# Kernel optimization log

Measured on AMD Instinct MI355X. Metric: run time of the kernel, lower is better.

The kernel has to match this reference:

```python
import jax, jax.numpy as jnp
import numpy as np
import math

# Model dims (from init_kwargs + mamba_ssm Mamba2 defaults)
D_MODEL = 1024
EXPAND = 2
HEADDIM = 64
D_STATE = 64
D_CONV = 4
NGROUPS = 1
D_INNER = EXPAND * D_MODEL            # 2048
NHEADS = D_INNER // HEADDIM           # 32
CONV_DIM = D_INNER + 2 * NGROUPS * D_STATE   # 2176
D_IN_PROJ = 2 * D_INNER + 2 * NGROUPS * D_STATE + NHEADS  # 4256
BATCH, SEQLEN = 4, 2048
RMS_EPS = 1.1920929e-07   # torch.finfo(float32).eps (nn.RMSNorm eps=None)
GNORM_EPS = 1e-5          # mamba_ssm RMSNormGated eps


def _rmsnorm(x, w, eps):
    return x * jax.lax.rsqrt(jnp.mean(x * x, axis=-1, keepdims=True) + eps) * w


def setup_inputs() -> dict:
    key = jax.random.key(0)
    ks = jax.random.split(key, 8)
    x = jax.random.normal(ks[0], (BATCH, SEQLEN, D_MODEL), jnp.float32)
    # router MLP (Linear(d_model,32) -> SiLU -> Linear(32,3))
    r_w1 = jax.random.normal(ks[1], (32, D_MODEL), jnp.float32) / math.sqrt(D_MODEL)
    r_b1 = jnp.zeros((32,), jnp.float32)
    r_w2 = jax.random.normal(ks[2], (3, 32), jnp.float32) / math.sqrt(32)
    r_b2 = jnp.zeros((3,), jnp.float32)
    # Mamba2 params
    in_proj_w = jax.random.normal(ks[3], (D_IN_PROJ, D_MODEL), jnp.float32) / math.sqrt(D_MODEL)
    conv_w = jax.random.normal(ks[4], (CONV_DIM, D_CONV), jnp.float32) * 0.2
    conv_b = jnp.zeros((CONV_DIM,), jnp.float32)
    dt_bias = jax.random.normal(ks[5], (NHEADS,), jnp.float32) * 0.1
    # OrthoSSM multi-scale override: A_log[i] = log(0.001 * 2**i)
    A_log = jnp.log(0.001 * (2.0 ** jnp.arange(NHEADS, dtype=jnp.float32)))
    D_param = jnp.ones((NHEADS,), jnp.float32)
    gnorm_w = jnp.ones((D_INNER,), jnp.float32)
    out_proj_w = jax.random.normal(ks[6], (D_MODEL, D_INNER), jnp.float32) / math.sqrt(D_INNER)
    norm_w = jnp.ones((D_MODEL,), jnp.float32)
    return {"x": x, "norm_w": norm_w, "r_w1": r_w1, "r_b1": r_b1, "r_w2": r_w2,
            "r_b2": r_b2, "in_proj_w": in_proj_w, "conv_w": conv_w, "conv_b": conv_b,
            "dt_bias": dt_bias, "A_log": A_log, "D_param": D_param,
            "gnorm_w": gnorm_w, "out_proj_w": out_proj_w}


def _forward(x, norm_w, r_w1, r_b1, r_w2, r_b2, in_proj_w, conv_w, conv_b,
             dt_bias, A_log, D_param, gnorm_w, out_proj_w):
    B, S, Dm = x.shape
    x_norm = _rmsnorm(x, norm_w, RMS_EPS)
    # --- router: mean-pool -> tiny MLP -> softmax over 3 tiers ---
    h = jax.nn.silu(x_norm.mean(axis=1) @ r_w1.T + r_b1)
    probs = jax.nn.softmax(h @ r_w2.T + r_b2, axis=-1)   # [B,3]
    p_fast = probs[:, 0][:, None, None]
    p_mamba = (probs[:, 1] + probs[:, 2])[:, None, None]
    # --- Mamba2(x_norm) ---
    zxbcdt = x_norm @ in_proj_w.T                         # [B,S,4256]
    z, xBC, dt = jnp.split(zxbcdt, [D_INNER, D_INNER + CONV_DIM], axis=-1)
    # causal depthwise conv1d (kernel 4) + SiLU
    conv = jax.lax.conv_general_dilated(
        xBC.transpose(0, 2, 1), conv_w[:, None, :], (1,), [(D_CONV - 1, 0)],
        feature_group_count=CONV_DIM)                      # [B,CONV_DIM,S]
    xBC = jax.nn.silu(conv.transpose(0, 2, 1) + conv_b)    # [B,S,CONV_DIM]
    xh, Bmat, Cmat = jnp.split(xBC, [D_INNER, D_INNER + NGROUPS * D_STATE], axis=-1)
    xh = xh.reshape(B, S, NHEADS, HEADDIM)                 # [B,S,H,P]
    dt = jax.nn.softplus(dt + dt_bias)                     # [B,S,H]
    A = -jnp.exp(A_log)                                    # [H]
    dA = jnp.exp(dt * A)                                   # [B,S,H]

    def step(hstate, inp):
        dA_t, dt_t, x_t, B_t, C_t = inp
        # hstate: [B,H,P,N]
        hstate = hstate * dA_t[..., None, None] \
                 + (dt_t[..., None] * x_t)[..., None] * B_t[:, None, None, :]
        y_t = jnp.einsum('bhpn,bn->bhp', hstate, C_t)
        return hstate, y_t

    h0 = jnp.zeros((B, NHEADS, HEADDIM, D_STATE), x.dtype)
    xs = (dA.transpose(1, 0, 2), dt.transpose(1, 0, 2), xh.transpose(1, 0, 2, 3),
          Bmat.transpose(1, 0, 2), Cmat.transpose(1, 0, 2))
    _, ys = jax.lax.scan(step, h0, xs)                     # [S,B,H,P]
    y = ys.transpose(1, 0, 2, 3) + D_param[:, None] * xh   # D skip connection
    y = y.reshape(B, S, D_INNER)
    # gated RMSNorm: norm(y * silu(z)) * weight
    yg = y * jax.nn.silu(z)
    yg = _rmsnorm(yg, gnorm_w, GNORM_EPS)
    mamba_out = yg @ out_proj_w.T                          # [B,S,D]
    out = p_fast * x_norm + p_mamba * mamba_out
    return x + out


def reference(x, norm_w, r_w1, r_b1, r_w2, r_b2, in_proj_w, conv_w, conv_b,
              dt_bias, A_log, D_param, gnorm_w, out_proj_w):
    return _forward(x, norm_w, r_w1, r_b1, r_w2, r_b2, in_proj_w, conv_w, conv_b,
                    dt_bias, A_log, D_param, gnorm_w, out_proj_w)
```

## Files before the change

### kernel.cpp

```cpp
#include <hip/hip_runtime.h>
#include <math.h>

typedef __bf16 bf16;
typedef __bf16 bf16x8 __attribute__((ext_vector_type(8)));
typedef __bf16 bf16x4 __attribute__((ext_vector_type(4)));
typedef float f32x4 __attribute__((ext_vector_type(4)));

#define DEV static __device__ __forceinline__
#define AS1 __attribute__((address_space(1)))
#define AS3 __attribute__((address_space(3)))

constexpr int kBatch = 4, kSeq = 2048, kDModel = 1024;
constexpr int kDInner = 2048, kHeads = 32;
constexpr int kConvDim = 2176, kDInProj = 4256, kNPad1 = 4352;
constexpr int kRows = kBatch * kSeq;
constexpr int kChunk = 64, kNChunk = kSeq / kChunk;
constexpr float kRmsEps = 1.1920929e-07f;
constexpr float kGnEps = 1e-5f;

DEV float siluf(float x) { return x / (1.f + expf(-x)); }

DEV float block_reduce_sum(float v, float* red, int tid) {
#pragma unroll
  for (int m = 1; m < 64; m <<= 1) v += __shfl_xor(v, m);
  if ((tid & 63) == 0) red[tid >> 6] = v;
  __syncthreads();
  return red[0] + red[1] + red[2] + red[3];
}

__global__ __launch_bounds__(256) void k_rmsnorm(const float* __restrict__ x,
                                                 const float* __restrict__ nw,
                                                 bf16* __restrict__ xnb,
                                                 float* __restrict__ rs) {
  const int row = blockIdx.x;
  const int tid = threadIdx.x;
  float4 v = ((const float4*)(x + (size_t)row * kDModel))[tid];
  __shared__ float red[4];
  float ss = block_reduce_sum(v.x * v.x + v.y * v.y + v.z * v.z + v.w * v.w, red, tid);
  float scale = rsqrtf(ss * (1.f / kDModel) + kRmsEps);
  if (tid == 0) rs[row] = scale;
  float4 wv = ((const float4*)nw)[tid];
  bf16x4 ov;
  ov[0] = (bf16)(v.x * scale * wv.x);
  ov[1] = (bf16)(v.y * scale * wv.y);
  ov[2] = (bf16)(v.z * scale * wv.z);
  ov[3] = (bf16)(v.w * scale * wv.w);
  *(bf16x4*)(xnb + (size_t)row * kDModel + tid * 4) = ov;
}

__global__ __launch_bounds__(128) void k_pool1(const bf16* __restrict__ xnb,
                                               float* __restrict__ part) {
  const int g = blockIdx.x, b = blockIdx.y;
  const int tid = threadIdx.x;
  const bf16* base = xnb + ((size_t)b * kSeq + (size_t)g * 32) * kDModel + tid * 8;
  float acc[8] = {0, 0, 0, 0, 0, 0, 0, 0};
  for (int r = 0; r < 32; ++r) {
    bf16x8 v = *(const bf16x8*)(base + (size_t)r * kDModel);
#pragma unroll
    for (int j = 0; j < 8; ++j) acc[j] += (float)v[j];
  }
  float* o = part + ((size_t)b * 64 + g) * kDModel + tid * 8;
#pragma unroll
  for (int j = 0; j < 8; ++j) o[j] = acc[j];
}

__global__ __launch_bounds__(256) void k_pool2(const float* __restrict__ part,
                                               float* __restrict__ mean) {
  const int idx = blockIdx.x * 256 + threadIdx.x;
  const int b = idx >> 10, d = idx & 1023;
  float s = 0.f;
  for (int g = 0; g < 64; ++g) s += part[((size_t)b * 64 + g) * kDModel + d];
  mean[idx] = s * (1.f / kSeq);
}

__global__ __launch_bounds__(128) void k_router(const float* __restrict__ mean,
                                                const float* __restrict__ w1,
                                                const float* __restrict__ b1,
                                                const float* __restrict__ w2,
                                                const float* __restrict__ b2,
                                                float* __restrict__ pfm) {
  __shared__ float hbuf[4][32];
  __shared__ float logit[4][3];
  const int t = threadIdx.x;
  {
    int b = t >> 5, j = t & 31;
    float s = b1[j];
    for (int d = 0; d < kDModel; ++d) s += mean[b * kDModel + d] * w1[j * kDModel + d];
    hbuf[b][j] = siluf(s);
  }
  __syncthreads();
  if (t < 12) {
    int b = t / 3, k = t % 3;
    float s = b2[k];
    for (int j = 0; j < 32; ++j) s += hbuf[b][j] * w2[k * 32 + j];
    logit[b][k] = s;
  }
  __syncthreads();
  if (t < 4) {
    float m = fmaxf(logit[t][0], fmaxf(logit[t][1], logit[t][2]));
    float e0 = expf(logit[t][0] - m), e1 = expf(logit[t][1] - m), e2 = expf(logit[t][2] - m);
    float inv = 1.f / (e0 + e1 + e2);
    pfm[t] = e0 * inv;
    pfm[4 + t] = (e1 + e2) * inv;
  }
}

__global__ __launch_bounds__(256) void k_castpad_w1(const float* __restrict__ w,
                                                    bf16* __restrict__ wb) {
  const size_t idx = (size_t)blockIdx.x * 256 + threadIdx.x;
  const int row = (int)(idx >> 10);
  wb[idx] = (bf16)(row < kDInProj ? w[idx] : 0.f);
}

__global__ __launch_bounds__(256) void k_cast_w2(const float* __restrict__ w,
                                                 const float* __restrict__ gw,
                                                 bf16* __restrict__ wb) {
  const size_t i4 = (size_t)blockIdx.x * 256 + threadIdx.x;
  const int k4 = (int)((i4 * 4) & (kDInner - 1));
  float4 v = ((const float4*)w)[i4];
  float4 g = *(const float4*)(gw + k4);
  bf16x4 o;
  o[0] = (bf16)(v.x * g.x); o[1] = (bf16)(v.y * g.y);
  o[2] = (bf16)(v.z * g.z); o[3] = (bf16)(v.w * g.w);
  ((bf16x4*)wb)[i4] = o;
}

template <int WM, int WN, int NF, bool FUSE>
__global__ __launch_bounds__(WM * WN * 64, 4) void k_gemm(
    const bf16* __restrict__ A, const bf16* __restrict__ B,
    bf16* __restrict__ Cb, const float* __restrict__ xres,
    const float* __restrict__ rs, const float* __restrict__ nw,
    const float* __restrict__ pfm, const float* __restrict__ rs2,
    float* __restrict__ outf, int K, int Nreal, int ldc, int ntn) {
  constexpr int THREADS = WM * WN * 64;
  constexpr int BM = WM * 64;
  constexpr int BN = WN * NF * 16;
  constexpr int NA = (BM * 4) / THREADS;
  constexpr int NB = (BN * 4) / THREADS;
  constexpr int ASZ = (BM / 2) * 64;
  constexpr int BSZ = (BN / 2) * 64;
  __shared__ __align__(16) bf16 lds[2 * ASZ + 2 * BSZ];
  const int tid = threadIdx.x;
  const int lane = tid & 63, wid = tid >> 6;
  const int wr = wid / WN, wc = wid % WN;
  const int lr = lane & 15, kb = lane >> 4;
  const int cpx = (int)gridDim.x >> 3;
  const int bid = ((int)blockIdx.x & 7) * cpx + ((int)blockIdx.x >> 3);
  const long n0 = (long)(bid % ntn) * BN;
  const long m0 = (long)(bid / ntn) * BM;

  f32x4 acc[4][NF];
#pragma unroll
  for (int i = 0; i < 4; ++i)
#pragma unroll
    for (int j = 0; j < NF; ++j) acc[i][j] = (f32x4){0.f, 0.f, 0.f, 0.f};

  const int nkt = K >> 5;

#define STAGE(pp, kt)                                                          \
  {                                                                            \
    const long koff = (long)(kt)*32;                                           \
    _Pragma("unroll") for (int j = 0; j < NA; ++j) {                           \
      int idx = j * THREADS + tid;                                             \
      int line = idx >> 3, sp = (idx & 7) ^ (line & 7);                        \
      int row = line * 2 + (sp >> 2), ch = sp & 3;                             \
      __builtin_amdgcn_global_load_lds(                                        \
          (const AS1 void*)(A + (m0 + row) * K + koff + ch * 8),               \
          (AS3 void*)((char*)(lds + (pp)*ASZ) + idx * 16), 16, 0, 0);          \
    }                                                                          \
    _Pragma("unroll") for (int j = 0; j < NB; ++j) {                           \
      int idx = j * THREADS + tid;                                             \
      int line = idx >> 3, sp = (idx & 7) ^ (line & 7);                        \
      int row = line * 2 + (sp >> 2), ch = sp & 3;                             \
      __builtin_amdgcn_global_load_lds(                                        \
          (const AS1 void*)(B + (n0 + row) * K + koff + ch * 8),               \
          (AS3 void*)((char*)(lds + 2 * ASZ + (pp)*BSZ) + idx * 16), 16, 0, 0);\
    }                                                                          \
  }
#define LOFF(r) (((r) >> 1) * 128 + (((((r)&1) << 2) | kb) ^ (((r) >> 1) & 7)) * 16)
#define RDA(pp, r) (*(const bf16x8*)((const char*)(lds + (pp)*ASZ) + LOFF(r)))
#define RDB(pp, r) (*(const bf16x8*)((const char*)(lds + 2 * ASZ + (pp)*BSZ) + LOFF(r)))

  bf16x8 bfr[NF];
  bf16x8 af[2];

  STAGE(0, 0);
  __syncthreads();
#pragma unroll
  for (int nf = 0; nf < NF; ++nf) bfr[nf] = RDB(0, wc * 64 + nf * 16 + lr);
  af[0] = RDA(0, wr * 64 + lr);

  for (int t = 0; t < nkt; ++t) {
    const int p = t & 1;
    if (t + 1 < nkt) STAGE(p ^ 1, t + 1);
#pragma unroll
    for (int q = 0; q < 4; ++q) {
      if (q < 3) af[(q + 1) & 1] = RDA(p, wr * 64 + (q + 1) * 16 + lr);
      __builtin_amdgcn_s_setprio(1);
#pragma unroll
      for (int nf = 0; nf < NF; ++nf)
        acc[q][nf] = __builtin_amdgcn_mfma_f32_16x16x32_bf16(af[q & 1], bfr[nf],
                                                             acc[q][nf], 0, 0, 0);
      __builtin_amdgcn_s_setprio(0);
    }
    if (t + 1 < nkt) {
      __syncthreads();
#pragma unroll
      for (int nf = 0; nf < NF; ++nf) bfr[nf] = RDB(p ^ 1, wc * 64 + nf * 16 + lr);
      af[0] = RDA(p ^ 1, wr * 64 + lr);
    }
  }
#undef STAGE
#undef LOFF
#undef RDA
#undef RDB

  const int rr = kb * 4;
  if constexpr (FUSE) {
    const int bx = (int)(m0 >> 11);
    const float pf = pfm[bx], pm = pfm[4 + bx];
#pragma unroll
    for (int mf = 0; mf < 4; ++mf) {
      long rbase = m0 + wr * 64 + mf * 16 + rr;
      float rsv[4], r2v[4];
#pragma unroll
      for (int j = 0; j < 4; ++j) { rsv[j] = rs[rbase + j]; r2v[j] = rs2[rbase + j]; }
#pragma unroll
      for (int nf = 0; nf < NF; ++nf) {
        int col = (int)n0 + wc * 64 + nf * 16 + lr;
        float wv = nw[col];
#pragma unroll
        for (int j = 0; j < 4; ++j) {
          size_t oi = (size_t)(rbase + j) * kDModel + col;
          float xv = xres[oi];
          outf[oi] = xv + pf * xv * rsv[j] * wv + pm * r2v[j] * acc[mf][nf][j];
        }
      }
    }
  } else {
    __syncthreads();
    bf16* scr = lds + wid * (16 * 72);
    const int srow = lane >> 2, cg = lane & 3;
#pragma unroll
    for (int mf = 0; mf < 4; ++mf) {
#pragma unroll
      for (int nf = 0; nf < NF; ++nf)
#pragma unroll
        for (int j = 0; j < 4; ++j)
          scr[(rr + j) * 72 + nf * 16 + lr] = (bf16)acc[mf][nf][j];
      asm volatile("s_waitcnt lgkmcnt(0)" ::: "memory");
      __builtin_amdgcn_sched_barrier(0);
      int col = (int)n0 + wc * (NF * 16) + cg * 16;
      if (col < Nreal) {
        long grow = m0 + wr * 64 + mf * 16 + srow;
        bf16x8 v0 = *(const bf16x8*)(scr + srow * 72 + cg * 16);
        bf16x8 v1 = *(const bf16x8*)(scr + srow * 72 + cg * 16 + 8);
        *(bf16x8*)(Cb + grow * (long)ldc + col) = v0;
        *(bf16x8*)(Cb + grow * (long)ldc + col + 8) = v1;
      }
      __builtin_amdgcn_sched_barrier(0);
    }
  }
}

__global__ __launch_bounds__(256) void k_conv(const bf16* __restrict__ zx,
                                              const float* __restrict__ cw,
                                              const float* __restrict__ cb,
                                              bf16* __restrict__ xbc) {
  const int gid = blockIdx.x * 256 + threadIdx.x;
  if (gid >= kRows * 272) return;
  const int row = gid / 272;
  const int cg = gid - row * 272;
  const int c0 = cg * 8;
  const int s = row & (kSeq - 1);
  const bf16* base = zx + (size_t)row * kDInProj + kDInner + c0;
  bf16x8 z8 = {};
  bf16x8 r3 = *(const bf16x8*)(base);
  bf16x8 r2 = (s >= 1) ? *(const bf16x8*)(base - kDInProj) : z8;
  bf16x8 r1 = (s >= 2) ? *(const bf16x8*)(base - 2 * kDInProj) : z8;
  bf16x8 r0 = (s >= 3) ? *(const bf16x8*)(base - 3 * kDInProj) : z8;
  bf16x8 o;
#pragma unroll
  for (int e = 0; e < 8; ++e) {
    float4 w = ((const float4*)cw)[c0 + e];
    float a = cb[c0 + e] + w.x * (float)r0[e] + w.y * (float)r1[e] +
              w.z * (float)r2[e] + w.w * (float)r3[e];
    o[e] = (bf16)siluf(a);
  }
  *(bf16x8*)(xbc + (size_t)row * kConvDim + c0) = o;
}

__global__ __launch_bounds__(256) void k_dtda(const bf16* __restrict__ zx,
                                              const float* __restrict__ dt_bias,
                                              const float* __restrict__ A_log,
                                              float* __restrict__ dt, float* __restrict__ ldA) {
  const int gid = blockIdx.x * 256 + threadIdx.x;
  const int row = gid >> 2, grp = gid & 3;
  bf16x8 r8 = *(const bf16x8*)(zx + (size_t)row * kDInProj + (kDInner + kConvDim) + grp * 8);
#pragma unroll
  for (int e = 0; e < 8; ++e) {
    int hh = grp * 8 + e;
    float raw = (float)r8[e] + dt_bias[hh];
    float dtv = (raw > 20.f) ? raw : log1pf(expf(raw));
    dt[row * kHeads + hh] = dtv;
    ldA[row * kHeads + hh] = dtv * -expf(A_log[hh]);
  }
}

__global__ __launch_bounds__(256) void k_chunkA(
    const bf16* __restrict__ xbc, const float* __restrict__ dtb,
    const float* __restrict__ ldab, float* __restrict__ cumbuf,
    float* __restrict__ Tc, bf16* __restrict__ yb, bf16* __restrict__ Sbuf) {
  const int c = blockIdx.x, h = blockIdx.y, b = blockIdx.z;
  const int tid = threadIdx.x;
  const int w = tid >> 6, lane = tid & 63, lr = lane & 15, kb = lane >> 4;
  const int rr = kb * 4;
  const int t0 = c * kChunk;
  __shared__ bf16 Bl[64 * 72], Cl[64 * 72], XT[64 * 72], WBT[64 * 72], Ml[64 * 72];
  __shared__ float cum_s[64], dt_s[64], w_s[64];

  {
    int s = tid >> 2, q = tid & 3;
    const bf16* rowp = xbc + ((size_t)b * kSeq + t0 + s) * kConvDim;
    bf16x8 x0 = *(const bf16x8*)(rowp + h * 64 + q * 16);
    bf16x8 x1 = *(const bf16x8*)(rowp + h * 64 + q * 16 + 8);
    bf16x8 b0 = *(const bf16x8*)(rowp + kDInner + q * 16);
    bf16x8 b1 = *(const bf16x8*)(rowp + kDInner + q * 16 + 8);
    bf16x8 c0 = *(const bf16x8*)(rowp + kDInner + 64 + q * 16);
    bf16x8 c1 = *(const bf16x8*)(rowp + kDInner + 64 + q * 16 + 8);
    *(bf16x8*)(Bl + s * 72 + q * 16) = b0;
    *(bf16x8*)(Bl + s * 72 + q * 16 + 8) = b1;
    *(bf16x8*)(Cl + s * 72 + q * 16) = c0;
    *(bf16x8*)(Cl + s * 72 + q * 16 + 8) = c1;
#pragma unroll
    for (int e = 0; e < 8; ++e) XT[(q * 16 + e) * 72 + s] = x0[e];
#pragma unroll
    for (int e = 0; e < 8; ++e) XT[(q * 16 + 8 + e) * 72 + s] = x1[e];
  }
  if (tid < 64) {
    size_t di = ((size_t)b * kSeq + t0 + tid) * kHeads + h;
    float v = ldab[di];
    float dtv = dtb[di];
#pragma unroll
    for (int o = 1; o < 64; o <<= 1) {
      float u = __shfl_up(v, o);
      if (lane >= o) v += u;
    }
    cum_s[tid] = v;
    dt_s[tid] = dtv;
    float tot = __shfl(v, 63);
    w_s[tid] = expf(tot - v) * dtv;
    cumbuf[(((size_t)b * kHeads + h) * kNChunk + c) * 64 + tid] = v;
    if (tid == 63) Tc[(b * kHeads + h) * kNChunk + c] = expf(v);
  }
  __syncthreads();

#pragma unroll
  for (int i = 0; i < 16; ++i) {
    int e = i * 256 + tid;
    int n = e >> 6, s = e & 63;
    WBT[n * 72 + s] = (bf16)((float)Bl[s * 72 + n] * w_s[s]);
  }

  f32x4 g[4];
#pragma unroll
  for (int nt = 0; nt < 4; ++nt) g[nt] = (f32x4){0.f, 0.f, 0.f, 0.f};
#pragma unroll
  for (int kk = 0; kk < 2; ++kk) {
    bf16x8 a = *(const bf16x8*)(Cl + (w * 16 + lr) * 72 + kk * 32 + kb * 8);
#pragma unroll
    for (int nt = 0; nt < 4; ++nt) {
      bf16x8 bb = *(const bf16x8*)(Bl + (nt * 16 + lr) * 72 + kk * 32 + kb * 8);
      g[nt] = __builtin_amdgcn_mfma_f32_16x16x32_bf16(a, bb, g[nt], 0, 0, 0);
    }
  }
#pragma unroll
  for (int nt = 0; nt < 4; ++nt)
#pragma unroll
    for (int j = 0; j < 4; ++j) {
      int tt = w * 16 + rr + j, ss = nt * 16 + lr;
      float m = (ss <= tt) ? g[nt][j] * expf(cum_s[tt] - cum_s[ss]) * dt_s[ss] : 0.f;
      Ml[tt * 72 + ss] = (bf16)m;
    }
  __syncthreads();

  f32x4 y4[4];
#pragma unroll
  for (int pt = 0; pt < 4; ++pt) y4[pt] = (f32x4){0.f, 0.f, 0.f, 0.f};
#pragma unroll
  for (int kk = 0; kk < 2; ++kk) {
    bf16x8 a = *(const bf16x8*)(Ml + (w * 16 + lr) * 72 + kk * 32 + kb * 8);
#pragma unroll
    for (int pt = 0; pt < 4; ++pt) {
      bf16x8 bb = *(const bf16x8*)(XT + (pt * 16 + lr) * 72 + kk * 32 + kb * 8);
      y4[pt] = __builtin_amdgcn_mfma_f32_16x16x32_bf16(a, bb, y4[pt], 0, 0, 0);
    }
  }
  f32x4 s4[4];
#pragma unroll
  for (int nt = 0; nt < 4; ++nt) s4[nt] = (f32x4){0.f, 0.f, 0.f, 0.f};
#pragma unroll
  for (int kk = 0; kk < 2; ++kk) {
    bf16x8 a = *(const bf16x8*)(XT + (w * 16 + lr) * 72 + kk * 32 + kb * 8);
#pragma unroll
    for (int nt = 0; nt < 4; ++nt) {
      bf16x8 bb = *(const bf16x8*)(WBT + (nt * 16 + lr) * 72 + kk * 32 + kb * 8);
      s4[nt] = __builtin_amdgcn_mfma_f32_16x16x32_bf16(a, bb, s4[nt], 0, 0, 0);
    }
  }
  __syncthreads();
#pragma unroll
  for (int pt = 0; pt < 4; ++pt)
#pragma unroll
    for (int j = 0; j < 4; ++j)
      Ml[(w * 16 + rr + j) * 72 + pt * 16 + lr] = (bf16)y4[pt][j];
  __syncthreads();
  {
    int row = tid >> 2, cg = tid & 3;
    bf16x8 v0 = *(const bf16x8*)(Ml + row * 72 + cg * 16);
    bf16x8 v1 = *(const bf16x8*)(Ml + row * 72 + cg * 16 + 8);
    bf16* dst = yb + ((size_t)b * kSeq + t0 + row) * kDInner + h * 64 + cg * 16;
    *(bf16x8*)dst = v0;
    *(bf16x8*)(dst + 8) = v1;
  }
  __syncthreads();
#pragma unroll
  for (int nt = 0; nt < 4; ++nt)
#pragma unroll
    for (int j = 0; j < 4; ++j)
      Ml[(w * 16 + rr + j) * 72 + nt * 16 + lr] = (bf16)s4[nt][j];
  __syncthreads();
  {
    int row = tid >> 2, cg = tid & 3;
    const size_t sbase = (((size_t)b * kHeads + h) * kNChunk + c) * 4096;
    bf16x8 v0 = *(const bf16x8*)(Ml + row * 72 + cg * 16);
    bf16x8 v1 = *(const bf16x8*)(Ml + row * 72 + cg * 16 + 8);
    bf16* dst = Sbuf + sbase + row * 64 + cg * 16;
    *(bf16x8*)dst = v0;
    *(bf16x8*)(dst + 8) = v1;
  }
}

__global__ __launch_bounds__(256) void k_chunkB(bf16* __restrict__ S,
                                                const float* __restrict__ Tc) {
  const int gid = blockIdx.x * 256 + threadIdx.x;
  const int bh = gid >> 10;
  const int pn = (gid & 1023) << 2;
  bf16* base = S + (size_t)bh * kNChunk * 4096 + pn;
  const float* tc = Tc + bh * kNChunk;
  float4 hh = {0.f, 0.f, 0.f, 0.f};
  bf16x4 s = *(const bf16x4*)(base);
  for (int c = 0; c < kNChunk; ++c) {
    bf16x4 sn = {};
    if (c + 1 < kNChunk) sn = *(const bf16x4*)(base + (size_t)(c + 1) * 4096);
    float t = tc[c];
    bf16x4 ho;
    ho[0] = (bf16)hh.x; ho[1] = (bf16)hh.y; ho[2] = (bf16)hh.z; ho[3] = (bf16)hh.w;
    *(bf16x4*)(base + (size_t)c * 4096) = ho;
    hh.x = t * hh.x + (float)s[0];
    hh.y = t * hh.y + (float)s[1];
    hh.z = t * hh.z + (float)s[2];
    hh.w = t * hh.w + (float)s[3];
    s = sn;
  }
}

__global__ __launch_bounds__(256) void k_chunkC(
    const bf16* __restrict__ xbc, const bf16* __restrict__ zx,
    const float* __restrict__ cumbuf, const bf16* __restrict__ hs,
    const float* __restrict__ Dp, bf16* __restrict__ yb) {
  const int c = blockIdx.x, h = blockIdx.y, b = blockIdx.z;
  const int tid = threadIdx.x;
  const int w = tid >> 6, lane = tid & 63, lr = lane & 15, kb = lane >> 4;
  const int rr = kb * 4;
  const int t0 = c * kChunk;
  __shared__ bf16 Cl[64 * 72];
  __shared__ float ecum[64];
  __shared__ float scrf[64 * 68];
  {
    int s = tid >> 2, q = tid & 3;
    const bf16* rowp = xbc + ((size_t)b * kSeq + t0 + s) * kConvDim + kDInner + 64 + q * 16;
    *(bf16x8*)(Cl + s * 72 + q * 16) = *(const bf16x8*)rowp;
    *(bf16x8*)(Cl + s * 72 + q * 16 + 8) = *(const bf16x8*)(rowp + 8);
  }
  if (tid < 64)
    ecum[tid] = expf(cumbuf[(((size_t)b * kHeads + h) * kNChunk + c) * 64 + tid]);
  __syncthreads();

  const bf16* hbase = hs + (((size_t)b * kHeads + h) * kNChunk + c) * 4096;
  f32x4 acc[4];
#pragma unroll
  for (int pt = 0; pt < 4; ++pt) acc[pt] = (f32x4){0.f, 0.f, 0.f, 0.f};
#pragma unroll
  for (int kk = 0; kk < 2; ++kk) {
    bf16x8 a = *(const bf16x8*)(Cl + (w * 16 + lr) * 72 + kk * 32 + kb * 8);
#pragma unroll
    for (int pt = 0; pt < 4; ++pt) {
      bf16x8 bb = *(const bf16x8*)(hbase + (pt * 16 + lr) * 64 + kk * 32 + kb * 8);
      acc[pt] = __builtin_amdgcn_mfma_f32_16x16x32_bf16(a, bb, acc[pt], 0, 0, 0);
    }
  }
#pragma unroll
  for (int pt = 0; pt < 4; ++pt)
#pragma unroll
    for (int j = 0; j < 4; ++j) {
      int tt = w * 16 + rr + j;
      scrf[tt * 68 + pt * 16 + lr] = ecum[tt] * acc[pt][j];
    }
  __syncthreads();
  {
    const float Dh = Dp[h];
    int row = tid >> 2, cg = tid & 3;
    size_t ri = (size_t)b * kSeq + t0 + row;
    const float* sp = scrf + row * 68 + cg * 16;
    bf16* yp = yb + ri * kDInner + h * 64 + cg * 16;
    const bf16* xp = xbc + ri * kConvDim + h * 64 + cg * 16;
    const bf16* zp = zx + ri * kDInProj + h * 64 + cg * 16;
#pragma unroll
    for (int half = 0; half < 2; ++half) {
      bf16x8 yv = *(const bf16x8*)(yp + half * 8);
      bf16x8 xv = *(const bf16x8*)(xp + half * 8);
      bf16x8 zv = *(const bf16x8*)(zp + half * 8);
      bf16x8 o;
#pragma unroll
      for (int e = 0; e < 8; ++e) {
        float yfull = (float)yv[e] + sp[half * 8 + e] + Dh * (float)xv[e];
        o[e] = (bf16)(yfull * siluf((float)zv[e]));
      }
      *(bf16x8*)(yp + half * 8) = o;
    }
  }
}

__global__ __launch_bounds__(256) void k_rowss(const bf16* __restrict__ g,
                                               float* __restrict__ rs2) {
  const int row = blockIdx.x;
  const int tid = threadIdx.x;
  bf16x8 v = *(const bf16x8*)(g + (size_t)row * kDInner + tid * 8);
  float ss = 0.f;
#pragma unroll
  for (int j = 0; j < 8; ++j) {
    float f = (float)v[j];
    ss += f * f;
  }
  __shared__ float red[4];
  ss = block_reduce_sum(ss, red, tid);
  if (tid == 0) rs2[row] = rsqrtf(ss * (1.f / kDInner) + kGnEps);
}

extern "C" void kernel_launch(void* const* d_in, const int* in_sizes, int n_in,
                              void* d_out, int out_size, void* d_ws, size_t ws_size,
                              hipStream_t stream) {
  const float* x = (const float*)d_in[0];
  const float* norm_w = (const float*)d_in[1];
  const float* r_w1 = (const float*)d_in[2];
  const float* r_b1 = (const float*)d_in[3];
  const float* r_w2 = (const float*)d_in[4];
  const float* r_b2 = (const float*)d_in[5];
  const float* in_proj_w = (const float*)d_in[6];
  const float* conv_w = (const float*)d_in[7];
  const float* conv_b = (const float*)d_in[8];
  const float* dt_bias = (const float*)d_in[9];
  const float* A_log = (const float*)d_in[10];
  const float* D_param = (const float*)d_in[11];
  const float* gnorm_w = (const float*)d_in[12];
  const float* out_proj_w = (const float*)d_in[13];
  float* out = (float*)d_out;
  char* ws = (char*)d_ws;

  bf16* xnb     = (bf16*)(ws + 0);
  bf16* w1b     = (bf16*)(ws + 16777216);
  bf16* zx      = (bf16*)(ws + 25690112);
  bf16* xbc     = (bf16*)(ws + 95420416);
  float* dtb    = (float*)(ws + 131072000);
  float* ldab   = (float*)(ws + 132120576);
  float* cumbuf = (float*)(ws + 133169152);
  float* Tcb    = (float*)(ws + 134217728);
  bf16* yb      = (bf16*)(ws + 134234112);
  bf16* Sbuf    = (bf16*)(ws + 167788544);
  bf16* w2b     = (bf16*)(ws + 201342976);
  float* part   = (float*)(ws + 205537280);
  float* meanb  = (float*)(ws + 206585856);
  float* pfm    = (float*)(ws + 206602240);
  float* rsb    = (float*)(ws + 206602368);
  float* rs2b   = (float*)(ws + 206635136);

  k_rmsnorm<<<kRows, 256, 0, stream>>>(x, norm_w, xnb, rsb);
  k_pool1<<<dim3(64, 4), 128, 0, stream>>>(xnb, part);
  k_pool2<<<16, 256, 0, stream>>>(part, meanb);
  k_router<<<1, 128, 0, stream>>>(meanb, r_w1, r_b1, r_w2, r_b2, pfm);
  k_castpad_w1<<<kNPad1 * kDModel / 256, 256, 0, stream>>>(in_proj_w, w1b);
  k_cast_w2<<<kDModel * kDInner / 1024, 256, 0, stream>>>(out_proj_w, gnorm_w, w2b);
  k_gemm<2, 4, 4, false><<<(kRows / 128) * (kNPad1 / 256), 512, 0, stream>>>(
      xnb, w1b, zx, nullptr, nullptr, nullptr, nullptr, nullptr, nullptr,
      kDModel, kDInProj, kDInProj, kNPad1 / 256);
  k_conv<<<kRows * 272 / 256, 256, 0, stream>>>(zx, conv_w, conv_b, xbc);
  k_dtda<<<kRows * 4 / 256, 256, 0, stream>>>(zx, dt_bias, A_log, dtb, ldab);
  k_chunkA<<<dim3(kNChunk, kHeads, kBatch), 256, 0, stream>>>(
      xbc, dtb, ldab, cumbuf, Tcb, yb, Sbuf);
  k_chunkB<<<512, 256, 0, stream>>>(Sbuf, Tcb);
  k_chunkC<<<dim3(kNChunk, kHeads, kBatch), 256, 0, stream>>>(
      xbc, zx, cumbuf, Sbuf, D_param, yb);
  k_rowss<<<kRows, 256, 0, stream>>>(yb, rs2b);
  k_gemm<2, 2, 4, true><<<(kRows / 128) * (kDModel / 128), 256, 0, stream>>>(
      yb, w2b, nullptr, x, rsb, norm_w, pfm, rs2b, out,
      kDInner, kDModel, kDModel, kDModel / 128);
}
```

Before: 361.3 us.

## Triple-buffer GEMM K-loop, fold row norm into out-proj GEMM, merge conv/dt kernels

The GEMM main loop moves from a double-buffered LDS pipeline to a three-stage one with explicit vmcnt waits and raw barriers, so global loads run further ahead of the MFMA work. The gated-RMSNorm sum of squares is now accumulated from the A fragments inside the fused out-projection GEMM, which removes the separate k_rowss pass over yb. The output GEMM tile shrinks to 64x128 with 128 threads to put more blocks on the device. k_conv and k_dtda are merged into one launch, and k_chunkA writes its two outputs through separate LDS buffers with fewer barriers. The trade-off is more LDS per block and a smaller output tile, which may reduce B reuse and occupancy.

```diff
diff --git a/kernel.cpp b/kernel.cpp
--- a/kernel.cpp
+++ b/kernel.cpp
@@ -130,16 +130,18 @@
     const bf16* __restrict__ A, const bf16* __restrict__ B,
     bf16* __restrict__ Cb, const float* __restrict__ xres,
     const float* __restrict__ rs, const float* __restrict__ nw,
-    const float* __restrict__ pfm, const float* __restrict__ rs2,
-    float* __restrict__ outf, int K, int Nreal, int ldc, int ntn) {
+    const float* __restrict__ pfm, float* __restrict__ outf,
+    int K, int Nreal, int ldc, int ntn) {
   constexpr int THREADS = WM * WN * 64;
   constexpr int BM = WM * 64;
   constexpr int BN = WN * NF * 16;
   constexpr int NA = (BM * 4) / THREADS;
   constexpr int NB = (BN * 4) / THREADS;
+  constexpr int VMN = NA + NB;
   constexpr int ASZ = (BM / 2) * 64;
   constexpr int BSZ = (BN / 2) * 64;
-  __shared__ __align__(16) bf16 lds[2 * ASZ + 2 * BSZ];
+  __shared__ __align__(16) bf16 lds[3 * ASZ + 3 * BSZ];
+  __shared__ float rs2s[BM];
   const int tid = threadIdx.x;
   const int lane = tid & 63, wid = tid >> 6;
   const int wr = wid / WN, wc = wid % WN;
@@ -154,6 +156,7 @@
   for (int i = 0; i < 4; ++i)
 #pragma unroll
     for (int j = 0; j < NF; ++j) acc[i][j] = (f32x4){0.f, 0.f, 0.f, 0.f};
+  float ssq[4] = {0.f, 0.f, 0.f, 0.f};
 
   const int nkt = K >> 5;
 
@@ -174,41 +177,62 @@
       int row = line * 2 + (sp >> 2), ch = sp & 3;                             \
       __builtin_amdgcn_global_load_lds(                                        \
           (const AS1 void*)(B + (n0 + row) * K + koff + ch * 8),               \
-          (AS3 void*)((char*)(lds + 2 * ASZ + (pp)*BSZ) + idx * 16), 16, 0, 0);\
+          (AS3 void*)((char*)(lds + 3 * ASZ + (pp)*BSZ) + idx * 16), 16, 0, 0);\
     }                                                                          \
   }
 #define LOFF(r) (((r) >> 1) * 128 + (((((r)&1) << 2) | kb) ^ (((r) >> 1) & 7)) * 16)
 #define RDA(pp, r) (*(const bf16x8*)((const char*)(lds + (pp)*ASZ) + LOFF(r)))
-#define RDB(pp, r) (*(const bf16x8*)((const char*)(lds + 2 * ASZ + (pp)*BSZ) + LOFF(r)))
-
-  bf16x8 bfr[NF];
-  bf16x8 af[2];
+#define RDB(pp, r) (*(const bf16x8*)((const char*)(lds + 3 * ASZ + (pp)*BSZ) + LOFF(r)))
 
   STAGE(0, 0);
-  __syncthreads();
-#pragma unroll
-  for (int nf = 0; nf < NF; ++nf) bfr[nf] = RDB(0, wc * 64 + nf * 16 + lr);
-  af[0] = RDA(0, wr * 64 + lr);
-
+  STAGE(1, 1);
+
+  int cur = 0;
   for (int t = 0; t < nkt; ++t) {
-    const int p = t & 1;
-    if (t + 1 < nkt) STAGE(p ^ 1, t + 1);
-#pragma unroll
-    for (int q = 0; q < 4; ++q) {
-      if (q < 3) af[(q + 1) & 1] = RDA(p, wr * 64 + (q + 1) * 16 + lr);
-      __builtin_amdgcn_s_setprio(1);
+    if (t + 2 < nkt) {
+      int sb = cur + 2; if (sb >= 3) sb -= 3;
+      STAGE(sb, t + 2);
+      if constexpr (VMN == 3) asm volatile("s_waitcnt vmcnt(6)" ::: "memory");
+      else if constexpr (VMN == 4) asm volatile("s_waitcnt vmcnt(8)" ::: "memory");
+      else asm volatile("s_waitcnt vmcnt(12)" ::: "memory");
+    } else if (t + 1 < nkt) {
+      if constexpr (VMN == 3) asm volatile("s_waitcnt vmcnt(3)" ::: "memory");
+      else if constexpr (VMN == 4) asm volatile("s_waitcnt vmcnt(4)" ::: "memory");
+      else asm volatile("s_waitcnt vmcnt(6)" ::: "memory");
+    } else {
+      asm volatile("s_waitcnt vmcnt(0)" ::: "memory");
+    }
+    __builtin_amdgcn_s_barrier();
+
+    bf16x8 af[4], bv[NF];
+#pragma unroll
+    for (int mf = 0; mf < 4; ++mf) af[mf] = RDA(cur, wr * 64 + mf * 16 + lr);
+#pragma unroll
+    for (int nf = 0; nf < NF; ++nf) bv[nf] = RDB(cur, wc * 64 + nf * 16 + lr);
+    asm volatile("s_waitcnt lgkmcnt(0)" ::: "memory");
+    __builtin_amdgcn_sched_barrier(0);
+    __builtin_amdgcn_s_barrier();
+
+    if constexpr (FUSE) {
+      if (wc == 0) {
+#pragma unroll
+        for (int mf = 0; mf < 4; ++mf)
+#pragma unroll
+          for (int e = 0; e < 8; ++e) {
+            float f = (float)af[mf][e];
+            ssq[mf] = fmaf(f, f, ssq[mf]);
+          }
+      }
+    }
+    __builtin_amdgcn_s_setprio(1);
+#pragma unroll
+    for (int mf = 0; mf < 4; ++mf)
 #pragma unroll
       for (int nf = 0; nf < NF; ++nf)
-        acc[q][nf] = __builtin_amdgcn_mfma_f32_16x16x32_bf16(af[q & 1], bfr[nf],
-                                                             acc[q][nf], 0, 0, 0);
-      __builtin_amdgcn_s_setprio(0);
-    }
-    if (t + 1 < nkt) {
-      __syncthreads();
-#pragma unroll
-      for (int nf = 0; nf < NF; ++nf) bfr[nf] = RDB(p ^ 1, wc * 64 + nf * 16 + lr);
-      af[0] = RDA(p ^ 1, wr * 64 + lr);
-    }
+        acc[mf][nf] = __builtin_amdgcn_mfma_f32_16x16x32_bf16(af[mf], bv[nf],
+                                                              acc[mf][nf], 0, 0, 0);
+    __builtin_amdgcn_s_setprio(0);
+    cur = cur + 1 == 3 ? 0 : cur + 1;
   }
 #undef STAGE
 #undef LOFF
@@ -217,6 +241,16 @@
 
   const int rr = kb * 4;
   if constexpr (FUSE) {
+    if (wc == 0) {
+#pragma unroll
+      for (int mf = 0; mf < 4; ++mf) {
+        float v = ssq[mf];
+        v += __shfl_xor(v, 16);
+        v += __shfl_xor(v, 32);
+        if (kb == 0) rs2s[wr * 64 + mf * 16 + lr] = rsqrtf(v * (1.f / kDInner) + kGnEps);
+      }
+    }
+    __syncthreads();
     const int bx = (int)(m0 >> 11);
     const float pf = pfm[bx], pm = pfm[4 + bx];
 #pragma unroll
@@ -224,7 +258,10 @@
       long rbase = m0 + wr * 64 + mf * 16 + rr;
       float rsv[4], r2v[4];
 #pragma unroll
-      for (int j = 0; j < 4; ++j) { rsv[j] = rs[rbase + j]; r2v[j] = rs2[rbase + j]; }
+      for (int j = 0; j < 4; ++j) {
+        rsv[j] = rs[rbase + j];
+        r2v[j] = rs2s[wr * 64 + mf * 16 + rr + j];
+      }
 #pragma unroll
       for (int nf = 0; nf < NF; ++nf) {
         int col = (int)n0 + wc * 64 + nf * 16 + lr;
@@ -263,47 +300,47 @@
   }
 }
 
-__global__ __launch_bounds__(256) void k_conv(const bf16* __restrict__ zx,
-                                              const float* __restrict__ cw,
-                                              const float* __restrict__ cb,
-                                              bf16* __restrict__ xbc) {
+__global__ __launch_bounds__(256) void k_convdt(const bf16* __restrict__ zx,
+                                                const float* __restrict__ cw,
+                                                const float* __restrict__ cb,
+                                                bf16* __restrict__ xbc,
+                                                const float* __restrict__ dt_bias,
+                                                const float* __restrict__ A_log,
+                                                float* __restrict__ dt,
+                                                float* __restrict__ ldA) {
   const int gid = blockIdx.x * 256 + threadIdx.x;
-  if (gid >= kRows * 272) return;
-  const int row = gid / 272;
-  const int cg = gid - row * 272;
-  const int c0 = cg * 8;
-  const int s = row & (kSeq - 1);
-  const bf16* base = zx + (size_t)row * kDInProj + kDInner + c0;
-  bf16x8 z8 = {};
-  bf16x8 r3 = *(const bf16x8*)(base);
-  bf16x8 r2 = (s >= 1) ? *(const bf16x8*)(base - kDInProj) : z8;
-  bf16x8 r1 = (s >= 2) ? *(const bf16x8*)(base - 2 * kDInProj) : z8;
-  bf16x8 r0 = (s >= 3) ? *(const bf16x8*)(base - 3 * kDInProj) : z8;
-  bf16x8 o;
-#pragma unroll
-  for (int e = 0; e < 8; ++e) {
-    float4 w = ((const float4*)cw)[c0 + e];
-    float a = cb[c0 + e] + w.x * (float)r0[e] + w.y * (float)r1[e] +
-              w.z * (float)r2[e] + w.w * (float)r3[e];
-    o[e] = (bf16)siluf(a);
-  }
-  *(bf16x8*)(xbc + (size_t)row * kConvDim + c0) = o;
-}
-
-__global__ __launch_bounds__(256) void k_dtda(const bf16* __restrict__ zx,
-                                              const float* __restrict__ dt_bias,
-                                              const float* __restrict__ A_log,
-                                              float* __restrict__ dt, float* __restrict__ ldA) {
-  const int gid = blockIdx.x * 256 + threadIdx.x;
-  const int row = gid >> 2, grp = gid & 3;
-  bf16x8 r8 = *(const bf16x8*)(zx + (size_t)row * kDInProj + (kDInner + kConvDim) + grp * 8);
-#pragma unroll
-  for (int e = 0; e < 8; ++e) {
-    int hh = grp * 8 + e;
-    float raw = (float)r8[e] + dt_bias[hh];
-    float dtv = (raw > 20.f) ? raw : log1pf(expf(raw));
-    dt[row * kHeads + hh] = dtv;
-    ldA[row * kHeads + hh] = dtv * -expf(A_log[hh]);
+  if (gid < kRows * 272) {
+    const int row = gid / 272;
+    const int cg = gid - row * 272;
+    const int c0 = cg * 8;
+    const int s = row & (kSeq - 1);
+    const bf16* base = zx + (size_t)row * kDInProj + kDInner + c0;
+    bf16x8 z8 = {};
+    bf16x8 r3 = *(const bf16x8*)(base);
+    bf16x8 r2 = (s >= 1) ? *(const bf16x8*)(base - kDInProj) : z8;
+    bf16x8 r1 = (s >= 2) ? *(const bf16x8*)(base - 2 * kDInProj) : z8;
+    bf16x8 r0 = (s >= 3) ? *(const bf16x8*)(base - 3 * kDInProj) : z8;
+    bf16x8 o;
+#pragma unroll
+    for (int e = 0; e < 8; ++e) {
+      float4 w = ((const float4*)cw)[c0 + e];
+      float a = cb[c0 + e] + w.x * (float)r0[e] + w.y * (float)r1[e] +
+                w.z * (float)r2[e] + w.w * (float)r3[e];
+      o[e] = (bf16)siluf(a);
+    }
+    *(bf16x8*)(xbc + (size_t)row * kConvDim + c0) = o;
+  } else {
+    const int g2 = gid - kRows * 272;
+    const int row = g2 >> 2, grp = g2 & 3;
+    bf16x8 r8 = *(const bf16x8*)(zx + (size_t)row * kDInProj + (kDInner + kConvDim) + grp * 8);
+#pragma unroll
+    for (int e = 0; e < 8; ++e) {
+      int hh = grp * 8 + e;
+      float raw = (float)r8[e] + dt_bias[hh];
+      float dtv = (raw > 20.f) ? raw : log1pf(expf(raw));
+      dt[row * kHeads + hh] = dtv;
+      ldA[row * kHeads + hh] = dtv * -expf(A_log[hh]);
+    }
   }
 }
 
@@ -408,36 +445,27 @@
       s4[nt] = __builtin_amdgcn_mfma_f32_16x16x32_bf16(a, bb, s4[nt], 0, 0, 0);
     }
   }
-  __syncthreads();
 #pragma unroll
   for (int pt = 0; pt < 4; ++pt)
 #pragma unroll
-    for (int j = 0; j < 4; ++j)
-      Ml[(w * 16 + rr + j) * 72 + pt * 16 + lr] = (bf16)y4[pt][j];
+    for (int j = 0; j < 4; ++j) {
+      Bl[(w * 16 + rr + j) * 72 + pt * 16 + lr] = (bf16)y4[pt][j];
+      Cl[(w * 16 + rr + j) * 72 + pt * 16 + lr] = (bf16)s4[pt][j];
+    }
   __syncthreads();
   {
     int row = tid >> 2, cg = tid & 3;
-    bf16x8 v0 = *(const bf16x8*)(Ml + row * 72 + cg * 16);
-    bf16x8 v1 = *(const bf16x8*)(Ml + row * 72 + cg * 16 + 8);
+    bf16x8 v0 = *(const bf16x8*)(Bl + row * 72 + cg * 16);
+    bf16x8 v1 = *(const bf16x8*)(Bl + row * 72 + cg * 16 + 8);
     bf16* dst = yb + ((size_t)b * kSeq + t0 + row) * kDInner + h * 64 + cg * 16;
     *(bf16x8*)dst = v0;
     *(bf16x8*)(dst + 8) = v1;
-  }
-  __syncthreads();
-#pragma unroll
-  for (int nt = 0; nt < 4; ++nt)
-#pragma unroll
-    for (int j = 0; j < 4; ++j)
-      Ml[(w * 16 + rr + j) * 72 + nt * 16 + lr] = (bf16)s4[nt][j];
-  __syncthreads();
-  {
-    int row = tid >> 2, cg = tid & 3;
     const size_t sbase = (((size_t)b * kHeads + h) * kNChunk + c) * 4096;
-    bf16x8 v0 = *(const bf16x8*)(Ml + row * 72 + cg * 16);
-    bf16x8 v1 = *(const bf16x8*)(Ml + row * 72 + cg * 16 + 8);
-    bf16* dst = Sbuf + sbase + row * 64 + cg * 16;
-    *(bf16x8*)dst = v0;
-    *(bf16x8*)(dst + 8) = v1;
+    bf16x8 u0 = *(const bf16x8*)(Cl + row * 72 + cg * 16);
+    bf16x8 u1 = *(const bf16x8*)(Cl + row * 72 + cg * 16 + 8);
+    bf16* sdst = Sbuf + sbase + row * 64 + cg * 16;
+    *(bf16x8*)sdst = u0;
+    *(bf16x8*)(sdst + 8) = u1;
   }
 }
 
@@ -532,22 +560,6 @@
   }
 }
 
-__global__ __launch_bounds__(256) void k_rowss(const bf16* __restrict__ g,
-                                               float* __restrict__ rs2) {
-  const int row = blockIdx.x;
-  const int tid = threadIdx.x;
-  bf16x8 v = *(const bf16x8*)(g + (size_t)row * kDInner + tid * 8);
-  float ss = 0.f;
-#pragma unroll
-  for (int j = 0; j < 8; ++j) {
-    float f = (float)v[j];
-    ss += f * f;
-  }
-  __shared__ float red[4];
-  ss = block_reduce_sum(ss, red, tid);
-  if (tid == 0) rs2[row] = rsqrtf(ss * (1.f / kDInner) + kGnEps);
-}
-
 extern "C" void kernel_launch(void* const* d_in, const int* in_sizes, int n_in,
                               void* d_out, int out_size, void* d_ws, size_t ws_size,
                               hipStream_t stream) {
@@ -583,7 +595,6 @@
   float* meanb  = (float*)(ws + 206585856);
   float* pfm    = (float*)(ws + 206602240);
   float* rsb    = (float*)(ws + 206602368);
-  float* rs2b   = (float*)(ws + 206635136);
 
   k_rmsnorm<<<kRows, 256, 0, stream>>>(x, norm_w, xnb, rsb);
   k_pool1<<<dim3(64, 4), 128, 0, stream>>>(xnb, part);
@@ -592,17 +603,16 @@
   k_castpad_w1<<<kNPad1 * kDModel / 256, 256, 0, stream>>>(in_proj_w, w1b);
   k_cast_w2<<<kDModel * kDInner / 1024, 256, 0, stream>>>(out_proj_w, gnorm_w, w2b);
   k_gemm<2, 4, 4, false><<<(kRows / 128) * (kNPad1 / 256), 512, 0, stream>>>(
-      xnb, w1b, zx, nullptr, nullptr, nullptr, nullptr, nullptr, nullptr,
+      xnb, w1b, zx, nullptr, nullptr, nullptr, nullptr, nullptr,
       kDModel, kDInProj, kDInProj, kNPad1 / 256);
-  k_conv<<<kRows * 272 / 256, 256, 0, stream>>>(zx, conv_w, conv_b, xbc);
-  k_dtda<<<kRows * 4 / 256, 256, 0, stream>>>(zx, dt_bias, A_log, dtb, ldab);
+  k_convdt<<<(kRows * 272 + kRows * 4) / 256, 256, 0, stream>>>(
+      zx, conv_w, conv_b, xbc, dt_bias, A_log, dtb, ldab);
   k_chunkA<<<dim3(kNChunk, kHeads, kBatch), 256, 0, stream>>>(
       xbc, dtb, ldab, cumbuf, Tcb, yb, Sbuf);
   k_chunkB<<<512, 256, 0, stream>>>(Sbuf, Tcb);
   k_chunkC<<<dim3(kNChunk, kHeads, kBatch), 256, 0, stream>>>(
       xbc, zx, cumbuf, Sbuf, D_param, yb);
-  k_rowss<<<kRows, 256, 0, stream>>>(yb, rs2b);
-  k_gemm<2, 2, 4, true><<<(kRows / 128) * (kDModel / 128), 256, 0, stream>>>(
-      yb, w2b, nullptr, x, rsb, norm_w, pfm, rs2b, out,
+  k_gemm<1, 2, 4, true><<<(kRows / 64) * (kDModel / 128), 128, 0, stream>>>(
+      yb, w2b, nullptr, x, rsb, norm_w, pfm, out,
       kDInner, kDModel, kDModel, kDModel / 128);
 }
```

Result: faster. 348.8 us (-3.5%).
